# Kernel tuning notes

Measured on AMD Instinct MI355X. Metric: run time of the kernel, lower is better.

## Reference

```python
import jax, jax.numpy as jnp
import numpy as np

N_NODES = 100000
N_EDGES = 1600000
DIM = 128


def setup_inputs() -> dict:
    key = jax.random.key(0)
    k1, k2, k3 = jax.random.split(key, 3)
    src = jax.random.randint(k1, (N_EDGES,), 0, N_NODES, dtype=jnp.int64 if jax.config.jax_enable_x64 else jnp.int32)
    # offset in [1, N) guarantees no self-loops (matches add_remaining_self_loops semantics cleanly)
    off = jax.random.randint(k2, (N_EDGES,), 1, N_NODES, dtype=src.dtype)
    dst = (src + off) % N_NODES
    edges = jnp.stack([src, dst], axis=1)  # [E, 2]
    x = jax.random.normal(k3, (N_NODES, DIM), dtype=jnp.float32)
    weight1 = jnp.ones((1, DIM), dtype=jnp.float32)
    bias1 = jnp.zeros((DIM,), dtype=jnp.float32)
    weight2 = jnp.ones((1, DIM), dtype=jnp.float32)
    bias2 = jnp.zeros((DIM,), dtype=jnp.float32)
    return {"edges": edges, "x": x, "weight1": weight1, "bias1": bias1,
            "weight2": weight2, "bias2": bias2}


def _gcn_norm(src_all, dst_all, num_nodes, dtype):
    # symmetric normalization: deg from row (src), norm_e = d^-1/2[src] * d^-1/2[dst]
    ones = jnp.ones(src_all.shape[0], dtype=dtype)
    deg = jax.ops.segment_sum(ones, src_all, num_segments=num_nodes)
    dinv = jnp.where(deg > 0, deg ** -0.5, 0.0).astype(dtype)
    return dinv[src_all] * dinv[dst_all]


def _gcn_layer(x, src_all, dst_all, norm, weight, bias):
    # GCNAlign_GCNConv: x = x * weight (elementwise, weight [1,D]);
    # out[i] = sum_{e: dst_e = i} norm_e * x[src_e]; then + bias
    x = x * weight
    msgs = norm[:, None] * x[src_all]          # [E+N, D] gather
    out = jax.ops.segment_sum(msgs, dst_all, num_segments=x.shape[0])  # scatter-add
    return out + bias


def reference(edges, x, weight1, bias1, weight2, bias2):
    num_nodes = x.shape[0]
    src, dst = edges[:, 0], edges[:, 1]
    loop = jnp.arange(num_nodes, dtype=src.dtype)
    src_all = jnp.concatenate([src, loop])
    dst_all = jnp.concatenate([dst, loop])
    norm = _gcn_norm(src_all, dst_all, num_nodes, x.dtype)
    # Encoder.forward (gcn-align, feat_drop=0): layer -> relu -> layer
    h = _gcn_layer(x, src_all, dst_all, norm, weight1, bias1)
    h = jax.nn.relu(h)
    h = _gcn_layer(h, src_all, dst_all, norm, weight2, bias2)
    return h
```

## Files before the change

### kernel.cpp

```cpp
#include <hip/hip_runtime.h>

#define DIM 128
#define EPB_A 8192
#define BSH 10
#define BNODES 1024
#define CAPB 18432
#define NBMAX 128

#if __has_builtin(__builtin_amdgcn_cvt_f32_ubyte0)
#define CVTU0 __builtin_amdgcn_cvt_f32_ubyte0
#define CVTU1 __builtin_amdgcn_cvt_f32_ubyte1
#define CVTU2 __builtin_amdgcn_cvt_f32_ubyte2
#define CVTU3 __builtin_amdgcn_cvt_f32_ubyte3
#else
__device__ __forceinline__ float CVTU0(unsigned u) { return (float)(u & 0xffu); }
__device__ __forceinline__ float CVTU1(unsigned u) { return (float)((u >> 8) & 0xffu); }
__device__ __forceinline__ float CVTU2(unsigned u) { return (float)((u >> 16) & 0xffu); }
__device__ __forceinline__ float CVTU3(unsigned u) { return (float)((u >> 24) & 0xffu); }
#endif


__global__ __launch_bounds__(512) void histscat(const int2* __restrict__ edges, int E,
                                                int* __restrict__ bcnt,
                                                int* __restrict__ scnt,
                                                unsigned* __restrict__ ebuck,
                                                unsigned short* __restrict__ sbuck,
                                                int NB) {
    __shared__ int hdst[NBMAX], hsrc[NBMAX], cdst[NBMAX], csrc[NBMAX];
    int tid = threadIdx.x;
    if (tid < NBMAX) { hdst[tid] = 0; hsrc[tid] = 0; }
    __syncthreads();
    int base = blockIdx.x * EPB_A;
    int cnt = min(EPB_A, E - base);
    int2 ed[16];
    #pragma unroll
    for (int i = 0; i < 16; ++i) {
        int idx = tid + i * 512;
        ed[i] = (idx < cnt) ? edges[base + idx] : make_int2(-1, -1);
    }
    #pragma unroll
    for (int i = 0; i < 16; ++i) {
        if (ed[i].x >= 0) {
            atomicAdd(&hdst[ed[i].y >> BSH], 1);
            atomicAdd(&hsrc[ed[i].x >> BSH], 1);
        }
    }
    __syncthreads();
    if (tid < NB) {
        if (hdst[tid] > 0) cdst[tid] = atomicAdd(&bcnt[tid], hdst[tid]);
        if (hsrc[tid] > 0) csrc[tid] = atomicAdd(&scnt[tid], hsrc[tid]);
    }
    __syncthreads();
    #pragma unroll
    for (int i = 0; i < 16; ++i) {
        if (ed[i].x >= 0) {
            int bd = ed[i].y >> BSH, bs = ed[i].x >> BSH;
            int p = atomicAdd(&cdst[bd], 1);
            ebuck[(size_t)bd * CAPB + p] =
                ((unsigned)ed[i].x << BSH) | (unsigned)(ed[i].y & (BNODES - 1));
            int q = atomicAdd(&csrc[bs], 1);
            sbuck[(size_t)bs * CAPB + q] = (unsigned short)(ed[i].x & (BNODES - 1));
        }
    }
}

__global__ __launch_bounds__(1024) void passD(const unsigned short* __restrict__ sbuck,
                                              const int* __restrict__ scnt,
                                              float* __restrict__ dinv, int N) {
    __shared__ int cnt[BNODES];
    int b = blockIdx.x, tid = threadIdx.x;
    int m = scnt[b];
    const unsigned short* sb = sbuck + (size_t)b * CAPB;
    cnt[tid] = 0;
    __syncthreads();
    for (int i = tid; i < m; i += 1024) atomicAdd(&cnt[sb[i]], 1);
    __syncthreads();
    int node = (b << BSH) + tid;
    if (node < N) dinv[node] = rsqrtf((float)(cnt[tid] + 1));
}

__global__ void conv_q8(const float4* __restrict__ xin, const float* __restrict__ dinv,
                        uint2* __restrict__ qx, float* __restrict__ scx, int n8) {
    int i = blockIdx.x * blockDim.x + threadIdx.x;
    if (i >= n8) return;
    int node = i >> 4, ln = i & 15;
    float dv = dinv[node];
    float4 v0 = xin[2 * i], v1 = xin[2 * i + 1];
    float y0 = dv * v0.x, y1 = dv * v0.y, y2 = dv * v0.z, y3 = dv * v0.w;
    float y4 = dv * v1.x, y5 = dv * v1.y, y6 = dv * v1.z, y7 = dv * v1.w;
    float mx = fmaxf(fmaxf(fmaxf(fabsf(y0), fabsf(y1)), fmaxf(fabsf(y2), fabsf(y3))),
                     fmaxf(fmaxf(fabsf(y4), fabsf(y5)), fmaxf(fabsf(y6), fabsf(y7))));
    mx = fmaxf(mx, __shfl_xor(mx, 1));
    mx = fmaxf(mx, __shfl_xor(mx, 2));
    mx = fmaxf(mx, __shfl_xor(mx, 4));
    mx = fmaxf(mx, __shfl_xor(mx, 8));
    float inv = (mx > 0.f) ? 127.f / mx : 0.f;
    unsigned q0 = (unsigned)(__float2int_rn(y0 * inv) + 128);
    unsigned q1 = (unsigned)(__float2int_rn(y1 * inv) + 128);
    unsigned q2 = (unsigned)(__float2int_rn(y2 * inv) + 128);
    unsigned q3 = (unsigned)(__float2int_rn(y3 * inv) + 128);
    unsigned q4 = (unsigned)(__float2int_rn(y4 * inv) + 128);
    unsigned q5 = (unsigned)(__float2int_rn(y5 * inv) + 128);
    unsigned q6 = (unsigned)(__float2int_rn(y6 * inv) + 128);
    unsigned q7 = (unsigned)(__float2int_rn(y7 * inv) + 128);
    uint2 ov;
    ov.x = q0 | (q1 << 8) | (q2 << 16) | (q3 << 24);
    ov.y = q4 | (q5 << 8) | (q6 << 16) | (q7 << 24);
    qx[(size_t)node * 16 + ln] = ov;
    if (ln == 0) scx[node] = mx * (1.f / 127.f);
}

__global__ __launch_bounds__(1024) void passC(const unsigned* __restrict__ ebuck,
                                              const int* __restrict__ bcnt,
                                              int* __restrict__ rowoff,
                                              int* __restrict__ csr_src,
                                              int N, int E, int NB) {
    __shared__ int cnt[BNODES];
    __shared__ int fill[BNODES];
    __shared__ int s[BNODES];
    __shared__ int red[128];
    int b = blockIdx.x, tid = threadIdx.x;
    if (tid < 128) red[tid] = (tid < NB && tid < b) ? bcnt[tid] : 0;
    __syncthreads();
    for (int off = 64; off > 0; off >>= 1) {
        if (tid < off) red[tid] += red[tid + off];
        __syncthreads();
    }
    int eb0 = red[0];
    int m = bcnt[b];
    const unsigned* eb = ebuck + (size_t)b * CAPB;
    cnt[tid] = 0;
    __syncthreads();
    for (int i = tid; i < m; i += 1024)
        atomicAdd(&cnt[eb[i] & (BNODES - 1u)], 1);
    __syncthreads();
    int node = (b << BSH) + tid;
    int val = (node < N) ? cnt[tid] + 1 : 0;
    s[tid] = val;
    __syncthreads();
    for (int off = 1; off < 1024; off <<= 1) {
        int t = (tid >= off) ? s[tid - off] : 0;
        __syncthreads();
        s[tid] += t;
        __syncthreads();
    }
    int excl = s[tid] - val;
    int csrb = eb0 + (b << BSH);
    if (node < N) rowoff[node] = csrb + excl;
    fill[tid] = excl;
    if (b == NB - 1 && tid == 0) rowoff[N] = E + N;
    __syncthreads();
    for (int i = tid; i < m; i += 1024) {
        unsigned u = eb[i];
        int p = atomicAdd(&fill[u & (BNODES - 1u)], 1);
        csr_src[csrb + p] = (int)(u >> BSH);
    }
    __syncthreads();
    if (node < N) csr_src[csrb + fill[tid]] = node;
}


#define ACCQ(r, sc) do {                                                   \
    a0 = fmaf(sc, CVTU0(r.x), a0); a1 = fmaf(sc, CVTU1(r.x), a1);          \
    a2 = fmaf(sc, CVTU2(r.x), a2); a3 = fmaf(sc, CVTU3(r.x), a3);          \
    a4 = fmaf(sc, CVTU0(r.y), a4); a5 = fmaf(sc, CVTU1(r.y), a5);          \
    a6 = fmaf(sc, CVTU2(r.y), a6); a7 = fmaf(sc, CVTU3(r.y), a7);          \
} while (0)

#define SLOT(j) do {                                                       \
    int  sj = __shfl(msrc, gb + (j));                                      \
    float sc = __shfl(msc, gb + (j));                                      \
    uint2 r = *(const uint2*)(qbase + (((unsigned)sj) << 7));              \
    ACCQ(r, sc);                                                           \
} while (0)

template<int BIASED, int LAST>
__global__ __launch_bounds__(256) void gcn_layer(
    const uint2* __restrict__ qin, const float* __restrict__ scin,
    const int* __restrict__ rowoff, const int* __restrict__ csr_src,
    const float* __restrict__ dinv,
    const float* __restrict__ w, const float* __restrict__ bia,
    void* __restrict__ qout, float* __restrict__ scout, int N) {
    int node = blockIdx.x * 4 + (threadIdx.x >> 6);
    if (node >= N) return;
    node = __builtin_amdgcn_readfirstlane(node);
    int lane = threadIdx.x & 63;
    int h  = lane >> 4;
    int ln = lane & 15;
    int gb = lane & 48;
    int start = rowoff[node];
    int mm = rowoff[node + 1] - start;
    float a0=0,a1=0,a2=0,a3=0,a4=0,a5=0,a6=0,a7=0;

    int off = h + 4 * ln;
    int offc = min(off, mm - 1);
    int  msrc = csr_src[start + offc];
    float msc = (off < mm) ? scin[msrc] : 0.f;

    const char* qbase = (const char*)qin + (ln << 3);

    SLOT(0); SLOT(1); SLOT(2); SLOT(3); SLOT(4); SLOT(5);
    if (__any(mm > 24)) {
        SLOT(6); SLOT(7); SLOT(8); SLOT(9); SLOT(10);
        SLOT(11); SLOT(12); SLOT(13); SLOT(14); SLOT(15);
    }
    float corr_t = 0.f;
    for (int o = 64 + h; o < mm; o += 4) {
        int sx = csr_src[start + o];
        float sc = scin[sx];
        uint2 c = *(const uint2*)(qbase + (((unsigned)sx) << 7));
        ACCQ(c, sc);
        if (BIASED && ln == 0) corr_t += sc;
    }

    a0+=__shfl_xor(a0,16); a1+=__shfl_xor(a1,16); a2+=__shfl_xor(a2,16); a3+=__shfl_xor(a3,16);
    a4+=__shfl_xor(a4,16); a5+=__shfl_xor(a5,16); a6+=__shfl_xor(a6,16); a7+=__shfl_xor(a7,16);
    a0+=__shfl_xor(a0,32); a1+=__shfl_xor(a1,32); a2+=__shfl_xor(a2,32); a3+=__shfl_xor(a3,32);
    a4+=__shfl_xor(a4,32); a5+=__shfl_xor(a5,32); a6+=__shfl_xor(a6,32); a7+=__shfl_xor(a7,32);

    if (BIASED) {
        float cv = msc + corr_t;
        cv += __shfl_xor(cv, 1);  cv += __shfl_xor(cv, 2);
        cv += __shfl_xor(cv, 4);  cv += __shfl_xor(cv, 8);
        cv += __shfl_xor(cv, 16); cv += __shfl_xor(cv, 32);
        float c = 128.f * cv;
        a0 -= c; a1 -= c; a2 -= c; a3 -= c; a4 -= c; a5 -= c; a6 -= c; a7 -= c;
    }

    if (h == 0) {
        float dn = dinv[node];
        float4 w0 = ((const float4*)w)[ln * 2],   w1 = ((const float4*)w)[ln * 2 + 1];
        float4 b0 = ((const float4*)bia)[ln * 2], b1 = ((const float4*)bia)[ln * 2 + 1];
        float o0 = fmaf(a0, dn * w0.x, b0.x), o1 = fmaf(a1, dn * w0.y, b0.y);
        float o2 = fmaf(a2, dn * w0.z, b0.z), o3 = fmaf(a3, dn * w0.w, b0.w);
        float o4 = fmaf(a4, dn * w1.x, b1.x), o5 = fmaf(a5, dn * w1.y, b1.y);
        float o6 = fmaf(a6, dn * w1.z, b1.z), o7 = fmaf(a7, dn * w1.w, b1.w);
        if (!LAST) {
            o0 = dn * fmaxf(o0, 0.f); o1 = dn * fmaxf(o1, 0.f);
            o2 = dn * fmaxf(o2, 0.f); o3 = dn * fmaxf(o3, 0.f);
            o4 = dn * fmaxf(o4, 0.f); o5 = dn * fmaxf(o5, 0.f);
            o6 = dn * fmaxf(o6, 0.f); o7 = dn * fmaxf(o7, 0.f);
            float mx = fmaxf(fmaxf(fmaxf(o0, o1), fmaxf(o2, o3)),
                             fmaxf(fmaxf(o4, o5), fmaxf(o6, o7)));
            mx = fmaxf(mx, __shfl_xor(mx, 1));
            mx = fmaxf(mx, __shfl_xor(mx, 2));
            mx = fmaxf(mx, __shfl_xor(mx, 4));
            mx = fmaxf(mx, __shfl_xor(mx, 8));
            float inv = (mx > 0.f) ? 255.f / mx : 0.f;
            unsigned q0 = (unsigned)__float2int_rn(o0 * inv);
            unsigned q1 = (unsigned)__float2int_rn(o1 * inv);
            unsigned q2 = (unsigned)__float2int_rn(o2 * inv);
            unsigned q3 = (unsigned)__float2int_rn(o3 * inv);
            unsigned q4 = (unsigned)__float2int_rn(o4 * inv);
            unsigned q5 = (unsigned)__float2int_rn(o5 * inv);
            unsigned q6 = (unsigned)__float2int_rn(o6 * inv);
            unsigned q7 = (unsigned)__float2int_rn(o7 * inv);
            uint2 ov;
            ov.x = q0 | (q1 << 8) | (q2 << 16) | (q3 << 24);
            ov.y = q4 | (q5 << 8) | (q6 << 16) | (q7 << 24);
            ((uint2*)qout)[(size_t)node * 16 + ln] = ov;
            if (ln == 0) scout[node] = mx * (1.f / 255.f);
        } else {
            ((float4*)qout)[(size_t)node * 32 + ln * 2]     = make_float4(o0, o1, o2, o3);
            ((float4*)qout)[(size_t)node * 32 + ln * 2 + 1] = make_float4(o4, o5, o6, o7);
        }
    }
}


static inline size_t align256(size_t x) { return (x + 255) & ~(size_t)255; }

extern "C" void kernel_launch(void* const* d_in, const int* in_sizes, int n_in,
                              void* d_out, int out_size, void* d_ws, size_t ws_size,
                              hipStream_t stream) {
    const int2*  edges = (const int2*)d_in[0];
    const float* x     = (const float*)d_in[1];
    const float* w1    = (const float*)d_in[2];
    const float* b1    = (const float*)d_in[3];
    const float* w2    = (const float*)d_in[4];
    const float* b2    = (const float*)d_in[5];
    float* out = (float*)d_out;

    const int E = in_sizes[0] / 2;
    const int N = in_sizes[1] / DIM;
    const int TOT = E + N;
    const int NB   = (N + BNODES - 1) >> BSH;
    const int nblk = (E + EPB_A - 1) / EPB_A;

    char* p = (char*)d_ws;
    int*            bcnt    = (int*)p;
    int*            scnt    = bcnt + NB;
    p += align256((size_t)2 * NB * 4);
    float*          dinv    = (float*)p;           p += align256((size_t)N * 4);
    float*          scX     = (float*)p;           p += align256((size_t)N * 4);
    float*          scH     = (float*)p;           p += align256((size_t)N * 4);
    int*            rowoff  = (int*)p;             p += align256((size_t)(N + 1) * 4);
    unsigned*       ebuck   = (unsigned*)p;        p += align256((size_t)NB * CAPB * 4);
    unsigned short* sbuck   = (unsigned short*)p;  p += align256((size_t)NB * CAPB * 2);
    int*            csr_src = (int*)p;             p += align256((size_t)TOT * 4);
    uint2*          qx      = (uint2*)p;           p += align256((size_t)N * DIM);
    uint2*          qh      = (uint2*)p;           p += align256((size_t)N * DIM);

    const int TPB = 256;
    int n8  = N * DIM / 8;
    int nbC = (n8 + TPB - 1) / TPB;

    hipMemsetAsync(bcnt, 0, (size_t)2 * NB * 4, stream);
    histscat<<<nblk, 512, 0, stream>>>(edges, E, bcnt, scnt, ebuck, sbuck, NB);
    passD<<<NB, 1024, 0, stream>>>(sbuck, scnt, dinv, N);
    conv_q8<<<nbC, TPB, 0, stream>>>((const float4*)x, dinv, qx, scX, n8);
    passC<<<NB, 1024, 0, stream>>>(ebuck, bcnt, rowoff, csr_src, N, E, NB);

    int nbL = (N + 3) / 4;
    gcn_layer<1, 0><<<nbL, TPB, 0, stream>>>(qx, scX, rowoff, csr_src, dinv,
                                             w1, b1, qh, scH, N);
    gcn_layer<0, 1><<<nbL, TPB, 0, stream>>>(qh, scH, rowoff, csr_src, dinv,
                                             w2, b2, out, nullptr, N);
}
```

Baseline: 166.5 us.

## Remap gather so each lane owns two features across all neighbours

Restructures the GCN aggregation kernel. The old version split each wavefront into four 16-lane groups that processed different edges on 8-byte rows and then reduced across groups with shuffles. Now every lane handles two feature bytes of a full 128-byte row and walks all neighbours, taking source indices through readlane. This drops the cross-group reduction and the h==0 epilogue divergence, so all lanes write output. The cost is more, smaller (2-byte) loads per edge and serial scale lookups per neighbour.

```diff
diff --git a/kernel.cpp b/kernel.cpp
--- a/kernel.cpp
+++ b/kernel.cpp
@@ -10,13 +10,9 @@
 #if __has_builtin(__builtin_amdgcn_cvt_f32_ubyte0)
 #define CVTU0 __builtin_amdgcn_cvt_f32_ubyte0
 #define CVTU1 __builtin_amdgcn_cvt_f32_ubyte1
-#define CVTU2 __builtin_amdgcn_cvt_f32_ubyte2
-#define CVTU3 __builtin_amdgcn_cvt_f32_ubyte3
 #else
 __device__ __forceinline__ float CVTU0(unsigned u) { return (float)(u & 0xffu); }
 __device__ __forceinline__ float CVTU1(unsigned u) { return (float)((u >> 8) & 0xffu); }
-__device__ __forceinline__ float CVTU2(unsigned u) { return (float)((u >> 16) & 0xffu); }
-__device__ __forceinline__ float CVTU3(unsigned u) { return (float)((u >> 24) & 0xffu); }
 #endif
 
 
@@ -160,23 +156,28 @@
 }
 
 
-#define ACCQ(r, sc) do {                                                   \
-    a0 = fmaf(sc, CVTU0(r.x), a0); a1 = fmaf(sc, CVTU1(r.x), a1);          \
-    a2 = fmaf(sc, CVTU2(r.x), a2); a3 = fmaf(sc, CVTU3(r.x), a3);          \
-    a4 = fmaf(sc, CVTU0(r.y), a4); a5 = fmaf(sc, CVTU1(r.y), a5);          \
-    a6 = fmaf(sc, CVTU2(r.y), a6); a7 = fmaf(sc, CVTU3(r.y), a7);          \
-} while (0)
-
-#define SLOT(j) do {                                                       \
-    int  sj = __shfl(msrc, gb + (j));                                      \
-    float sc = __shfl(msc, gb + (j));                                      \
-    uint2 r = *(const uint2*)(qbase + (((unsigned)sj) << 7));              \
-    ACCQ(r, sc);                                                           \
-} while (0)
+#define SLOT4(j)                                                              \
+    int s0 = __builtin_amdgcn_readlane(msrc, (j));                            \
+    int s1 = __builtin_amdgcn_readlane(msrc, (j) + 1);                        \
+    int s2 = __builtin_amdgcn_readlane(msrc, (j) + 2);                        \
+    int s3 = __builtin_amdgcn_readlane(msrc, (j) + 3);                        \
+    float c0 = scin[s0];                                                      \
+    float c1 = ((j) + 1 < mm) ? scin[s1] : 0.f;                               \
+    float c2 = ((j) + 2 < mm) ? scin[s2] : 0.f;                               \
+    float c3 = ((j) + 3 < mm) ? scin[s3] : 0.f;                               \
+    unsigned r0 = *(const unsigned short*)(qin + (((size_t)(unsigned)s0) << 7) + 2 * lane); \
+    unsigned r1 = *(const unsigned short*)(qin + (((size_t)(unsigned)s1) << 7) + 2 * lane); \
+    unsigned r2 = *(const unsigned short*)(qin + (((size_t)(unsigned)s2) << 7) + 2 * lane); \
+    unsigned r3 = *(const unsigned short*)(qin + (((size_t)(unsigned)s3) << 7) + 2 * lane); \
+    a0 = fmaf(c0, CVTU0(r0), a0); a1 = fmaf(c0, CVTU1(r0), a1);               \
+    a0 = fmaf(c1, CVTU0(r1), a0); a1 = fmaf(c1, CVTU1(r1), a1);               \
+    a0 = fmaf(c2, CVTU0(r2), a0); a1 = fmaf(c2, CVTU1(r2), a1);               \
+    a0 = fmaf(c3, CVTU0(r3), a0); a1 = fmaf(c3, CVTU1(r3), a1);               \
+    if (BIASED) corr += (c0 + c1) + (c2 + c3);
 
 template<int BIASED, int LAST>
 __global__ __launch_bounds__(256) void gcn_layer(
-    const uint2* __restrict__ qin, const float* __restrict__ scin,
+    const unsigned char* __restrict__ qin, const float* __restrict__ scin,
     const int* __restrict__ rowoff, const int* __restrict__ csr_src,
     const float* __restrict__ dinv,
     const float* __restrict__ w, const float* __restrict__ bia,
@@ -185,85 +186,52 @@
     if (node >= N) return;
     node = __builtin_amdgcn_readfirstlane(node);
     int lane = threadIdx.x & 63;
-    int h  = lane >> 4;
-    int ln = lane & 15;
-    int gb = lane & 48;
     int start = rowoff[node];
     int mm = rowoff[node + 1] - start;
-    float a0=0,a1=0,a2=0,a3=0,a4=0,a5=0,a6=0,a7=0;
-
-    int off = h + 4 * ln;
-    int offc = min(off, mm - 1);
-    int  msrc = csr_src[start + offc];
-    float msc = (off < mm) ? scin[msrc] : 0.f;
-
-    const char* qbase = (const char*)qin + (ln << 3);
-
-    SLOT(0); SLOT(1); SLOT(2); SLOT(3); SLOT(4); SLOT(5);
-    if (__any(mm > 24)) {
-        SLOT(6); SLOT(7); SLOT(8); SLOT(9); SLOT(10);
-        SLOT(11); SLOT(12); SLOT(13); SLOT(14); SLOT(15);
-    }
-    float corr_t = 0.f;
-    for (int o = 64 + h; o < mm; o += 4) {
-        int sx = csr_src[start + o];
+    int msrc = csr_src[start + min(lane, mm - 1)];
+    float a0 = 0.f, a1 = 0.f, corr = 0.f;
+
+    int nb = min((mm + 3) >> 2, 16);
+    for (int b = 0; b < nb; ++b) {
+        SLOT4(4 * b);
+    }
+    for (int o = 64; o < mm; ++o) {
+        int sx = __builtin_amdgcn_readfirstlane(csr_src[start + o]);
         float sc = scin[sx];
-        uint2 c = *(const uint2*)(qbase + (((unsigned)sx) << 7));
-        ACCQ(c, sc);
-        if (BIASED && ln == 0) corr_t += sc;
-    }
-
-    a0+=__shfl_xor(a0,16); a1+=__shfl_xor(a1,16); a2+=__shfl_xor(a2,16); a3+=__shfl_xor(a3,16);
-    a4+=__shfl_xor(a4,16); a5+=__shfl_xor(a5,16); a6+=__shfl_xor(a6,16); a7+=__shfl_xor(a7,16);
-    a0+=__shfl_xor(a0,32); a1+=__shfl_xor(a1,32); a2+=__shfl_xor(a2,32); a3+=__shfl_xor(a3,32);
-    a4+=__shfl_xor(a4,32); a5+=__shfl_xor(a5,32); a6+=__shfl_xor(a6,32); a7+=__shfl_xor(a7,32);
+        unsigned r = *(const unsigned short*)(qin + (((size_t)(unsigned)sx) << 7) + 2 * lane);
+        a0 = fmaf(sc, CVTU0(r), a0);
+        a1 = fmaf(sc, CVTU1(r), a1);
+        if (BIASED) corr += sc;
+    }
 
     if (BIASED) {
-        float cv = msc + corr_t;
-        cv += __shfl_xor(cv, 1);  cv += __shfl_xor(cv, 2);
-        cv += __shfl_xor(cv, 4);  cv += __shfl_xor(cv, 8);
-        cv += __shfl_xor(cv, 16); cv += __shfl_xor(cv, 32);
-        float c = 128.f * cv;
-        a0 -= c; a1 -= c; a2 -= c; a3 -= c; a4 -= c; a5 -= c; a6 -= c; a7 -= c;
-    }
-
-    if (h == 0) {
-        float dn = dinv[node];
-        float4 w0 = ((const float4*)w)[ln * 2],   w1 = ((const float4*)w)[ln * 2 + 1];
-        float4 b0 = ((const float4*)bia)[ln * 2], b1 = ((const float4*)bia)[ln * 2 + 1];
-        float o0 = fmaf(a0, dn * w0.x, b0.x), o1 = fmaf(a1, dn * w0.y, b0.y);
-        float o2 = fmaf(a2, dn * w0.z, b0.z), o3 = fmaf(a3, dn * w0.w, b0.w);
-        float o4 = fmaf(a4, dn * w1.x, b1.x), o5 = fmaf(a5, dn * w1.y, b1.y);
-        float o6 = fmaf(a6, dn * w1.z, b1.z), o7 = fmaf(a7, dn * w1.w, b1.w);
-        if (!LAST) {
-            o0 = dn * fmaxf(o0, 0.f); o1 = dn * fmaxf(o1, 0.f);
-            o2 = dn * fmaxf(o2, 0.f); o3 = dn * fmaxf(o3, 0.f);
-            o4 = dn * fmaxf(o4, 0.f); o5 = dn * fmaxf(o5, 0.f);
-            o6 = dn * fmaxf(o6, 0.f); o7 = dn * fmaxf(o7, 0.f);
-            float mx = fmaxf(fmaxf(fmaxf(o0, o1), fmaxf(o2, o3)),
-                             fmaxf(fmaxf(o4, o5), fmaxf(o6, o7)));
-            mx = fmaxf(mx, __shfl_xor(mx, 1));
-            mx = fmaxf(mx, __shfl_xor(mx, 2));
-            mx = fmaxf(mx, __shfl_xor(mx, 4));
-            mx = fmaxf(mx, __shfl_xor(mx, 8));
-            float inv = (mx > 0.f) ? 255.f / mx : 0.f;
-            unsigned q0 = (unsigned)__float2int_rn(o0 * inv);
-            unsigned q1 = (unsigned)__float2int_rn(o1 * inv);
-            unsigned q2 = (unsigned)__float2int_rn(o2 * inv);
-            unsigned q3 = (unsigned)__float2int_rn(o3 * inv);
-            unsigned q4 = (unsigned)__float2int_rn(o4 * inv);
-            unsigned q5 = (unsigned)__float2int_rn(o5 * inv);
-            unsigned q6 = (unsigned)__float2int_rn(o6 * inv);
-            unsigned q7 = (unsigned)__float2int_rn(o7 * inv);
-            uint2 ov;
-            ov.x = q0 | (q1 << 8) | (q2 << 16) | (q3 << 24);
-            ov.y = q4 | (q5 << 8) | (q6 << 16) | (q7 << 24);
-            ((uint2*)qout)[(size_t)node * 16 + ln] = ov;
-            if (ln == 0) scout[node] = mx * (1.f / 255.f);
-        } else {
-            ((float4*)qout)[(size_t)node * 32 + ln * 2]     = make_float4(o0, o1, o2, o3);
-            ((float4*)qout)[(size_t)node * 32 + ln * 2 + 1] = make_float4(o4, o5, o6, o7);
-        }
+        a0 = fmaf(-128.f, corr, a0);
+        a1 = fmaf(-128.f, corr, a1);
+    }
+
+    float dn = dinv[node];
+    float2 wv = ((const float2*)w)[lane];
+    float2 bv = ((const float2*)bia)[lane];
+    float o0 = fmaf(a0, dn * wv.x, bv.x);
+    float o1 = fmaf(a1, dn * wv.y, bv.y);
+    if (!LAST) {
+        o0 = dn * fmaxf(o0, 0.f);
+        o1 = dn * fmaxf(o1, 0.f);
+        float mx = fmaxf(o0, o1);
+        mx = fmaxf(mx, __shfl_xor(mx, 1));
+        mx = fmaxf(mx, __shfl_xor(mx, 2));
+        mx = fmaxf(mx, __shfl_xor(mx, 4));
+        mx = fmaxf(mx, __shfl_xor(mx, 8));
+        mx = fmaxf(mx, __shfl_xor(mx, 16));
+        mx = fmaxf(mx, __shfl_xor(mx, 32));
+        float inv = (mx > 0.f) ? 255.f / mx : 0.f;
+        unsigned q0 = (unsigned)__float2int_rn(o0 * inv);
+        unsigned q1 = (unsigned)__float2int_rn(o1 * inv);
+        *(unsigned short*)((unsigned char*)qout + (size_t)node * DIM + 2 * lane) =
+            (unsigned short)(q0 | (q1 << 8));
+        if (lane == 0) scout[node] = mx * (1.f / 255.f);
+    } else {
+        ((float2*)qout)[(size_t)node * 64 + lane] = make_float2(o0, o1);
     }
 }
 
@@ -298,8 +266,8 @@
     unsigned*       ebuck   = (unsigned*)p;        p += align256((size_t)NB * CAPB * 4);
     unsigned short* sbuck   = (unsigned short*)p;  p += align256((size_t)NB * CAPB * 2);
     int*            csr_src = (int*)p;             p += align256((size_t)TOT * 4);
-    uint2*          qx      = (uint2*)p;           p += align256((size_t)N * DIM);
-    uint2*          qh      = (uint2*)p;           p += align256((size_t)N * DIM);
+    unsigned char*  qx      = (unsigned char*)p;   p += align256((size_t)N * DIM);
+    unsigned char*  qh      = (unsigned char*)p;   p += align256((size_t)N * DIM);
 
     const int TPB = 256;
     int n8  = N * DIM / 8;
@@ -308,7 +276,7 @@
     hipMemsetAsync(bcnt, 0, (size_t)2 * NB * 4, stream);
     histscat<<<nblk, 512, 0, stream>>>(edges, E, bcnt, scnt, ebuck, sbuck, NB);
     passD<<<NB, 1024, 0, stream>>>(sbuck, scnt, dinv, N);
-    conv_q8<<<nbC, TPB, 0, stream>>>((const float4*)x, dinv, qx, scX, n8);
+    conv_q8<<<nbC, TPB, 0, stream>>>((const float4*)x, dinv, (uint2*)qx, scX, n8);
     passC<<<NB, 1024, 0, stream>>>(ebuck, bcnt, rowoff, csr_src, N, E, NB);
 
     int nbL = (N + 3) / 4;
```

Result: slower. 184.3 us (+10.6%).

## Store short adjacency lists in fixed-stride per-node padded CSR records

Applied to the files above, without the earlier changes.

passC now writes each node's degree and, for nodes with at most 24 entries (self-loop included), their source list into a fixed 25-int record per node. Long lists still go to the regular CSR. The layer kernel reads the count and sources from that one record, which removes the rowoff lookups and the dependent indexed CSR load for the common low-degree case. In exchange it adds a strided per-node buffer that spreads each node's edge writes in passC, plus a divergent branch in the layer kernel. Nodes whose lists go to the padded buffer leave their CSR slots unwritten.

```diff
diff --git a/kernel.cpp b/kernel.cpp
--- a/kernel.cpp
+++ b/kernel.cpp
@@ -6,6 +6,7 @@
 #define BNODES 1024
 #define CAPB 18432
 #define NBMAX 128
+#define PSTR 25
 
 #if __has_builtin(__builtin_amdgcn_cvt_f32_ubyte0)
 #define CVTU0 __builtin_amdgcn_cvt_f32_ubyte0
@@ -114,9 +115,11 @@
                                               const int* __restrict__ bcnt,
                                               int* __restrict__ rowoff,
                                               int* __restrict__ csr_src,
+                                              int* __restrict__ pcsr,
                                               int N, int E, int NB) {
     __shared__ int cnt[BNODES];
     __shared__ int fill[BNODES];
+    __shared__ int sbase[BNODES];
     __shared__ int s[BNODES];
     __shared__ int red[128];
     int b = blockIdx.x, tid = threadIdx.x;
@@ -146,17 +149,31 @@
     }
     int excl = s[tid] - val;
     int csrb = eb0 + (b << BSH);
-    if (node < N) rowoff[node] = csrb + excl;
+    if (node < N) {
+        rowoff[node] = csrb + excl;
+        pcsr[(size_t)node * PSTR] = val;
+    }
     fill[tid] = excl;
+    sbase[tid] = excl;
     if (b == NB - 1 && tid == 0) rowoff[N] = E + N;
     __syncthreads();
     for (int i = tid; i < m; i += 1024) {
         unsigned u = eb[i];
-        int p = atomicAdd(&fill[u & (BNODES - 1u)], 1);
-        csr_src[csrb + p] = (int)(u >> BSH);
-    }
-    __syncthreads();
-    if (node < N) csr_src[csrb + fill[tid]] = node;
+        int loc = (int)(u & (BNODES - 1u));
+        int p = atomicAdd(&fill[loc], 1);
+        int src = (int)(u >> BSH);
+        if (cnt[loc] <= 23) {
+            int gn = (b << BSH) + loc;
+            pcsr[(size_t)gn * PSTR + 1 + (p - sbase[loc])] = src;
+        } else {
+            csr_src[csrb + p] = src;
+        }
+    }
+    __syncthreads();
+    if (node < N) {
+        if (cnt[tid] <= 23) pcsr[(size_t)node * PSTR + 1 + cnt[tid]] = node;
+        else                csr_src[csrb + fill[tid]] = node;
+    }
 }
 
 
@@ -178,7 +195,7 @@
 __global__ __launch_bounds__(256) void gcn_layer(
     const uint2* __restrict__ qin, const float* __restrict__ scin,
     const int* __restrict__ rowoff, const int* __restrict__ csr_src,
-    const float* __restrict__ dinv,
+    const int* __restrict__ pcsr, const float* __restrict__ dinv,
     const float* __restrict__ w, const float* __restrict__ bia,
     void* __restrict__ qout, float* __restrict__ scout, int N) {
     int node = blockIdx.x * 4 + (threadIdx.x >> 6);
@@ -188,29 +205,35 @@
     int h  = lane >> 4;
     int ln = lane & 15;
     int gb = lane & 48;
-    int start = rowoff[node];
-    int mm = rowoff[node + 1] - start;
     float a0=0,a1=0,a2=0,a3=0,a4=0,a5=0,a6=0,a7=0;
-
+    const char* qbase = (const char*)qin + (ln << 3);
+
+    int mm = pcsr[(size_t)node * PSTR];
     int off = h + 4 * ln;
-    int offc = min(off, mm - 1);
-    int  msrc = csr_src[start + offc];
-    float msc = (off < mm) ? scin[msrc] : 0.f;
-
-    const char* qbase = (const char*)qin + (ln << 3);
-
-    SLOT(0); SLOT(1); SLOT(2); SLOT(3); SLOT(4); SLOT(5);
-    if (__any(mm > 24)) {
+    float msc;
+    int msrc;
+    float corr_t = 0.f;
+
+    if (mm <= 24) {
+        int v = pcsr[(size_t)node * PSTR + 1 + min(off, 23)];
+        msrc = min(max(v, 0), N - 1);
+        msc = (off < mm) ? scin[msrc] : 0.f;
+        SLOT(0); SLOT(1); SLOT(2); SLOT(3); SLOT(4); SLOT(5);
+    } else {
+        int start = rowoff[node];
+        int offc = min(off, mm - 1);
+        msrc = csr_src[start + offc];
+        msc = (off < mm) ? scin[msrc] : 0.f;
+        SLOT(0); SLOT(1); SLOT(2); SLOT(3); SLOT(4); SLOT(5);
         SLOT(6); SLOT(7); SLOT(8); SLOT(9); SLOT(10);
         SLOT(11); SLOT(12); SLOT(13); SLOT(14); SLOT(15);
-    }
-    float corr_t = 0.f;
-    for (int o = 64 + h; o < mm; o += 4) {
-        int sx = csr_src[start + o];
-        float sc = scin[sx];
-        uint2 c = *(const uint2*)(qbase + (((unsigned)sx) << 7));
-        ACCQ(c, sc);
-        if (BIASED && ln == 0) corr_t += sc;
+        for (int o = 64 + h; o < mm; o += 4) {
+            int sx = csr_src[start + o];
+            float sc = scin[sx];
+            uint2 c = *(const uint2*)(qbase + (((unsigned)sx) << 7));
+            ACCQ(c, sc);
+            if (BIASED && ln == 0) corr_t += sc;
+        }
     }
 
     a0+=__shfl_xor(a0,16); a1+=__shfl_xor(a1,16); a2+=__shfl_xor(a2,16); a3+=__shfl_xor(a3,16);
@@ -298,6 +321,7 @@
     unsigned*       ebuck   = (unsigned*)p;        p += align256((size_t)NB * CAPB * 4);
     unsigned short* sbuck   = (unsigned short*)p;  p += align256((size_t)NB * CAPB * 2);
     int*            csr_src = (int*)p;             p += align256((size_t)TOT * 4);
+    int*            pcsr    = (int*)p;             p += align256((size_t)N * PSTR * 4);
     uint2*          qx      = (uint2*)p;           p += align256((size_t)N * DIM);
     uint2*          qh      = (uint2*)p;           p += align256((size_t)N * DIM);
 
@@ -309,11 +333,11 @@
     histscat<<<nblk, 512, 0, stream>>>(edges, E, bcnt, scnt, ebuck, sbuck, NB);
     passD<<<NB, 1024, 0, stream>>>(sbuck, scnt, dinv, N);
     conv_q8<<<nbC, TPB, 0, stream>>>((const float4*)x, dinv, qx, scX, n8);
-    passC<<<NB, 1024, 0, stream>>>(ebuck, bcnt, rowoff, csr_src, N, E, NB);
+    passC<<<NB, 1024, 0, stream>>>(ebuck, bcnt, rowoff, csr_src, pcsr, N, E, NB);
 
     int nbL = (N + 3) / 4;
-    gcn_layer<1, 0><<<nbL, TPB, 0, stream>>>(qx, scX, rowoff, csr_src, dinv,
+    gcn_layer<1, 0><<<nbL, TPB, 0, stream>>>(qx, scX, rowoff, csr_src, pcsr, dinv,
                                              w1, b1, qh, scH, N);
-    gcn_layer<0, 1><<<nbL, TPB, 0, stream>>>(qh, scH, rowoff, csr_src, dinv,
+    gcn_layer<0, 1><<<nbL, TPB, 0, stream>>>(qh, scH, rowoff, csr_src, pcsr, dinv,
                                              w2, b2, out, nullptr, N);
 }
```

New measurement: 167.1 us. Within noise of the previous version (+0.3%).
